# Optimization experiments

Measured on AMD Instinct MI355X. Metric: run time of the kernel, lower is better.

## Reference

```python
import jax, jax.numpy as jnp
import numpy as np

N_POINTS = 2_000_000
N_BATCH = 8


def cart2polar(xyz):
    rho = jnp.sqrt(xyz[:, 0] ** 2 + xyz[:, 1] ** 2)
    phi = jnp.arctan2(xyz[:, 1], xyz[:, 0])
    return jnp.stack((rho, phi, xyz[:, 2]), axis=1)


def setup_inputs() -> dict:
    key = jax.random.key(0)
    k1, k2, k3, k4 = jax.random.split(key, 4)
    xy = jax.random.uniform(k1, (N_POINTS, 2), minval=-50.0, maxval=50.0)
    z = jax.random.uniform(k2, (N_POINTS, 1), minval=-4.0, maxval=2.0)
    inten = jax.random.uniform(k3, (N_POINTS, 1))
    points = jnp.concatenate([xy, z, inten], axis=1)  # [N, 4]
    batch_idx = jnp.sort(jax.random.randint(k4, (N_POINTS,), 0, N_BATCH)).astype(jnp.int32)
    coors_range_xyz = jnp.array([[0.0, 50.0], [-np.pi, np.pi], [-4.0, 2.0]], dtype=jnp.float32)
    spatial_shape = np.array([480, 360, 32])  # static
    scale_list = np.array([2, 4, 1])          # module appends 1; static
    return dict(points=points, batch_idx=batch_idx,
                coors_range_xyz=coors_range_xyz,
                spatial_shape=spatial_shape, scale_list=scale_list)


def _unique_rows(bxyz, dims):
    # Encode [b, gx, gy, gz] rows into a single int32 key (max 8*480*360*32 ~ 44M).
    key = ((bxyz[:, 0] * dims[0] + bxyz[:, 1]) * dims[1] + bxyz[:, 2]) * dims[2] + bxyz[:, 3]
    order = jnp.argsort(key)
    sk = key[order]
    flags = jnp.concatenate([jnp.ones((1,), bool), sk[1:] != sk[:-1]])
    rank = jnp.cumsum(flags.astype(jnp.int32)) - 1          # unique-id per sorted row
    inv = jnp.zeros_like(rank).at[order].set(rank)           # inverse map, like torch.unique
    # first occurrence of each unique row (all rows with same rank are identical)
    unq = jnp.zeros_like(bxyz).at[rank].set(bxyz[order])     # padded to [N, 4]
    num_unique = rank[-1] + 1
    return unq, inv, num_unique


def reference(points, batch_idx, coors_range_xyz, spatial_shape, scale_list):
    pc = points[:, :3]
    xyz_pol = cart2polar(pc)
    lo = coors_range_xyz[:, 0]
    hi = coors_range_xyz[:, 1]
    crop = hi - lo
    ss_np = np.asarray(spatial_shape)
    outs = []
    for scale in [int(s) for s in np.asarray(scale_list)]:
        cells = jnp.asarray(np.ceil(ss_np / scale) - 1.0, dtype=xyz_pol.dtype)
        grid = jnp.floor((jnp.clip(xyz_pol, lo, hi) - lo) / crop * cells).astype(jnp.int32)
        bxyz = jnp.concatenate([batch_idx[:, None].astype(jnp.int32), grid], axis=1)  # [N,4]
        dims = np.ceil(ss_np / scale).astype(np.int64)
        unq, inv, num = _unique_rows(bxyz, dims)
        # reorder unique coords as [b, z, y, x], cast int32 (torch: unq[:, [0,3,2,1]])
        coors = jnp.concatenate([unq[:, 0:1], unq[:, 3:4], unq[:, 2:3], unq[:, 1:2]], axis=1).astype(jnp.int32)
        outs.extend([bxyz, inv, coors, num])
    return tuple(outs)
```

## Files before the change

kernel.cpp:

```cpp
#include <hip/hip_runtime.h>
#include <cstdint>

#define DI __device__ __forceinline__

constexpr int NPTS       = 2000000;
constexpr int STRIDE_OUT = 18000001;
constexpr int OFF_INV    = 8000000;
constexpr int OFF_COORS  = 10000000;
constexpr int OFF_NUM    = 18000000;

constexpr int R2W  = 172800;
constexpr int R4W  = 21600;
constexpr int R1W  = 1382400;
constexpr int RW0  = 0;
constexpr int RW1  = R2W;
constexpr int RW2  = R2W + R4W;
constexpr int WTOT = R2W + R4W + R1W;
constexpr int NB1  = (WTOT + 1023) / 1024;
constexpr int J2   = 8;
constexpr int P1   = 6;
constexpr int J1   = 4;
constexpr int S1W  = 28800;
constexpr int S1BITS = S1W * 32;

constexpr int NBLK_INV   = (NPTS + 255) / 256;
constexpr int NBLK_INV8  = ((NBLK_INV + 7) / 8) * 8;
constexpr int INV_QUOT   = NBLK_INV8 / 8;
constexpr int NBLK_COORS = (WTOT + 255) / 256;
constexpr int NBLK_TAIL  = (3 * NPTS + 255) / 256;

DI float fmul_s(float a, float b){ float r; asm("v_mul_f32 %0, %1, %2" : "=v"(r) : "v"(a), "v"(b)); return r; }
DI float fadd_s(float a, float b){ float r; asm("v_add_f32 %0, %1, %2" : "=v"(r) : "v"(a), "v"(b)); return r; }

DI void compute_keys(float x, float y, float z, int b, int (&key)[3]) {
  const float PI_F     = 3.14159265358979323846f;
  const float TWO_PI_F = 6.28318530717958647692f;
  float rho = sqrtf(fadd_s(fmul_s(x, x), fmul_s(y, y)));
  float phi = atan2f(y, x);
  float tr = (fminf(fmaxf(rho, 0.0f), 50.0f) - 0.0f) / 50.0f;
  float tp = (fminf(fmaxf(phi, -PI_F), PI_F) + PI_F) / TWO_PI_F;
  float tz = (fminf(fmaxf(z, -4.0f), 2.0f) + 4.0f) / 6.0f;
  constexpr float C0[3] = {239.f, 119.f, 479.f};
  constexpr float C1[3] = {179.f,  89.f, 359.f};
  constexpr float C2[3] = { 15.f,   7.f,  31.f};
  constexpr int   D0[3] = {240, 120, 480};
  constexpr int   D1[3] = {180,  90, 360};
  constexpr int   D2[3] = { 16,   8,  32};
  #pragma unroll
  for (int s = 0; s < 3; ++s) {
    int a0 = (int)floorf(tr * C0[s]);
    int a1 = (int)floorf(tp * C1[s]);
    int a2 = (int)floorf(tz * C2[s]);
    key[s] = ((b * D0[s] + a0) * D1[s] + a1) * D2[s] + a2;
  }
}

__global__ __launch_bounds__(256) void pass_keys(const float4* __restrict__ pts,
                                                 const int* __restrict__ batch, int n,
                                                 int* __restrict__ keys,
                                                 int* __restrict__ bstart) {
  int i = blockIdx.x * 256 + threadIdx.x;
  if (i >= n) return;
  float4 p = pts[i];
  int bi = batch[i];
  int key[3];
  compute_keys(p.x, p.y, p.z, bi, key);
  keys[i] = key[0]; keys[n + i] = key[1]; keys[2 * n + i] = key[2];
  if (i == 0) {
    #pragma unroll 1
    for (int k = 0; k <= bi; ++k) bstart[k] = 0;
  }
  int bnext = (i + 1 < n) ? batch[i + 1] : 8;
  #pragma unroll 1
  for (int k = bi + 1; k <= bnext; ++k) bstart[k] = i + 1;
}

__global__ __launch_bounds__(1024) void hist_all(const int* __restrict__ bstart,
                                                 const int* __restrict__ keys, int n,
                                                 uint32_t* __restrict__ rep2s,
                                                 uint32_t* __restrict__ rep4s,
                                                 uint32_t* __restrict__ rep1s) {
  alignas(16) __shared__ uint32_t bmA[S1W];
  alignas(16) __shared__ uint32_t bmB[2700];
  int t = threadIdx.x;
  int pb = blockIdx.x;
  if (pb < 64) {
    int bv = pb & 7, j = pb >> 3;
    for (int w = t * 4; w < 21600; w += 4096) *reinterpret_cast<uint4*>(bmA + w) = make_uint4(0,0,0,0);
    for (int w = t; w < 2700; w += 1024) bmB[w] = 0;
    __syncthreads();
    int lo = bstart[bv];
    int hi = bstart[bv + 1];
    int sz = hi - lo;
    int s = lo + (int)((long long)sz * j / J2);
    int e = lo + (int)((long long)sz * (j + 1) / J2);
    const int* k0 = keys;
    const int* k1 = keys + n;
    for (int i = s + t; i < e; i += 1024) {
      int ink2 = k0[i] - bv * 691200;
      int ink4 = k1[i] - bv * 86400;
      atomicOr(&bmA[ink2 >> 5], 1u << (ink2 & 31));
      atomicOr(&bmB[ink4 >> 5], 1u << (ink4 & 31));
    }
    __syncthreads();
    uint32_t* d2 = rep2s + (size_t)j * R2W + bv * 21600;
    uint32_t* d4 = rep4s + (size_t)j * R4W + bv * 2700;
    for (int w = t * 4; w < 21600; w += 4096) *reinterpret_cast<uint4*>(d2 + w) = *reinterpret_cast<uint4*>(bmA + w);
    for (int w = t * 4; w < 2700; w += 4096) *reinterpret_cast<uint4*>(d4 + w) = *reinterpret_cast<uint4*>(bmB + w);
  } else {
    int bv = pb & 7;
    int id = (pb - 64) >> 3;
    int j = id / 6, r = id - j * 6;
    int slice = bv * 6 + r;
    for (int w = t * 4; w < S1W; w += 4096) *reinterpret_cast<uint4*>(bmA + w) = make_uint4(0,0,0,0);
    __syncthreads();
    int lo = bstart[bv];
    int hi = bstart[bv + 1];
    int sz = hi - lo;
    int s = lo + (int)((long long)sz * j / J1);
    int e = lo + (int)((long long)sz * (j + 1) / J1);
    const int* k2 = keys + 2 * n;
    int base = bv * 5529600 + r * S1BITS;
    for (int i = s + t; i < e; i += 1024) {
      int rel = k2[i] - base;
      if ((unsigned)rel < (unsigned)S1BITS) atomicOr(&bmA[rel >> 5], 1u << (rel & 31));
    }
    __syncthreads();
    uint32_t* d = rep1s + (size_t)j * R1W + (size_t)slice * S1W;
    for (int w = t * 4; w < S1W; w += 4096) *reinterpret_cast<uint4*>(d + w) = *reinterpret_cast<uint4*>(bmA + w);
  }
}

DI uint4 merged_words(int base, const uint32_t* __restrict__ rep2s,
                      const uint32_t* __restrict__ rep4s,
                      const uint32_t* __restrict__ rep1s) {
  uint4 acc = make_uint4(0, 0, 0, 0);
  if (base < RW1) {
    #pragma unroll
    for (int c = 0; c < J2; ++c) {
      uint4 w = *reinterpret_cast<const uint4*>(rep2s + (size_t)c * R2W + base);
      acc.x |= w.x; acc.y |= w.y; acc.z |= w.z; acc.w |= w.w;
    }
  } else if (base < RW2) {
    int l = base - RW1;
    #pragma unroll
    for (int c = 0; c < J2; ++c) {
      uint4 w = *reinterpret_cast<const uint4*>(rep4s + (size_t)c * R4W + l);
      acc.x |= w.x; acc.y |= w.y; acc.z |= w.z; acc.w |= w.w;
    }
  } else {
    int l = base - RW2;
    #pragma unroll
    for (int c = 0; c < J1; ++c) {
      uint4 w = *reinterpret_cast<const uint4*>(rep1s + (size_t)c * R1W + l);
      acc.x |= w.x; acc.y |= w.y; acc.z |= w.z; acc.w |= w.w;
    }
  }
  return acc;
}

__global__ __launch_bounds__(256) void scanA(const uint32_t* __restrict__ rep2s,
                                             const uint32_t* __restrict__ rep4s,
                                             const uint32_t* __restrict__ rep1s,
                                             uint32_t* __restrict__ bits,
                                             uint32_t* __restrict__ blockSums) {
  __shared__ uint32_t lds[256];
  int t = threadIdx.x;
  int base = blockIdx.x * 1024 + t * 4;
  uint32_t s = 0;
  if (base < WTOT) {
    uint4 m = merged_words(base, rep2s, rep4s, rep1s);
    *reinterpret_cast<uint4*>(bits + base) = m;
    s = __popc(m.x) + __popc(m.y) + __popc(m.z) + __popc(m.w);
  }
  lds[t] = s; __syncthreads();
  for (int off = 128; off > 0; off >>= 1) { if (t < off) lds[t] += lds[t + off]; __syncthreads(); }
  if (t == 0) blockSums[blockIdx.x] = lds[0];
}

__global__ __launch_bounds__(256) void scanC(const uint32_t* __restrict__ bits,
                                             const uint32_t* __restrict__ blockSums,
                                             uint2* __restrict__ pairs) {
  __shared__ uint32_t lds[256];
  int t = threadIdx.x;
  uint32_t bs = 0;
  for (int k = t; k < (int)blockIdx.x; k += 256) bs += blockSums[k];
  lds[t] = bs; __syncthreads();
  for (int off = 128; off > 0; off >>= 1) { if (t < off) lds[t] += lds[t + off]; __syncthreads(); }
  uint32_t blockBase = lds[0];
  __syncthreads();
  int base = blockIdx.x * 1024 + t * 4;
  uint32_t b[4] = {0,0,0,0}; uint32_t c[4]; uint32_t sum = 0;
  if (base < WTOT) {
    uint4 w = *reinterpret_cast<const uint4*>(bits + base);
    b[0] = w.x; b[1] = w.y; b[2] = w.z; b[3] = w.w;
  }
  #pragma unroll
  for (int k = 0; k < 4; ++k) { c[k] = __popc(b[k]); sum += c[k]; }
  lds[t] = sum; __syncthreads();
  for (int off = 1; off < 256; off <<= 1) {
    uint32_t x = (t >= off) ? lds[t - off] : 0u; __syncthreads();
    lds[t] += x; __syncthreads();
  }
  uint32_t excl = lds[t] - sum + blockBase;
  if (base < WTOT) {
    #pragma unroll
    for (int k = 0; k < 4; ++k) { pairs[base + k] = make_uint2(b[k], excl); excl += c[k]; }
  }
}

template <int S>
DI int4 decode_key(int key) {
  constexpr int D0[3] = {240, 120, 480};
  constexpr int D1[3] = {180,  90, 360};
  constexpr int D2[3] = { 16,   8,  32};
  int a2 = key & (D2[S] - 1);
  int r  = key / D2[S];
  int q  = r / D1[S];
  int a1 = r - q * D1[S];
  int b  = q / D0[S];
  int a0 = q - b * D0[S];
  return make_int4(b, a0, a1, a2);
}

template <int S>
DI void coors_word(int wi_local, uint32_t bits, uint32_t rank, int* __restrict__ coors) {
  int keybase = wi_local * 32;
  while (bits) {
    int j = __builtin_ctz(bits);
    bits &= bits - 1;
    int4 d = decode_key<S>(keybase + j);
    *reinterpret_cast<int4*>(coors + (size_t)rank * 4) = make_int4(d.x, d.w, d.z, d.y);
    ++rank;
  }
}

__global__ __launch_bounds__(256) void epilogue(int n, const uint2* __restrict__ pairs,
                                                const int* __restrict__ keys,
                                                int* __restrict__ out) {
  int b = blockIdx.x;
  int t = threadIdx.x;
  if (b < NBLK_INV8) {
    int l = (b & 7) * INV_QUOT + (b >> 3);
    if (l >= NBLK_INV) return;
    int i = l * 256 + t;
    if (i >= n) return;
    int key[3] = { keys[i], keys[n + i], keys[2 * n + i] };
    constexpr int RW[3] = {RW0, RW1, RW2};
    *reinterpret_cast<int4*>(out + 0 * STRIDE_OUT + i * 4) = decode_key<0>(key[0]);
    *reinterpret_cast<int4*>(out + 1 * STRIDE_OUT + i * 4) = decode_key<1>(key[1]);
    *reinterpret_cast<int4*>(out + 2 * STRIDE_OUT + i * 4) = decode_key<2>(key[2]);
    #pragma unroll
    for (int s = 0; s < 3; ++s) {
      uint2 pr = pairs[RW[s] + (key[s] >> 5)];
      uint32_t base = pr.y - ((s == 0) ? 0u : pairs[RW[s]].y);
      int rank = (int)(base + __popc(pr.x & ((1u << (key[s] & 31)) - 1u)));
      out[s * STRIDE_OUT + OFF_INV + i] = rank;
    }
  } else if (b < NBLK_INV8 + NBLK_COORS) {
    int wi = (b - NBLK_INV8) * 256 + t;
    if (wi >= WTOT) return;
    uint2 pr = pairs[wi];
    if (!pr.x) return;
    if (wi < RW1)      coors_word<0>(wi,       pr.x, pr.y,                 out + 0 * STRIDE_OUT + OFF_COORS);
    else if (wi < RW2) coors_word<1>(wi - RW1, pr.x, pr.y - pairs[RW1].y,  out + 1 * STRIDE_OUT + OFF_COORS);
    else               coors_word<2>(wi - RW2, pr.x, pr.y - pairs[RW2].y,  out + 2 * STRIDE_OUT + OFF_COORS);
  } else {
    int idx = (b - NBLK_INV8 - NBLK_COORS) * 256 + t;
    if (idx >= 3 * n) return;
    int s = 0, i = idx;
    if (i >= 2 * n)  { s = 2; i -= 2 * n; }
    else if (i >= n) { s = 1; i -= n; }
    uint2 last = pairs[WTOT - 1];
    uint32_t total = last.y + (uint32_t)__popc(last.x);
    uint32_t lo = (s == 0) ? 0u : pairs[(s == 1) ? RW1 : RW2].y;
    uint32_t hi = (s == 0) ? pairs[RW1].y : (s == 1) ? pairs[RW2].y : total;
    uint32_t num = hi - lo;
    if (i == 0) out[s * STRIDE_OUT + OFF_NUM] = (int)num;
    if ((uint32_t)i >= num)
      *reinterpret_cast<int4*>(out + s * STRIDE_OUT + OFF_COORS + (size_t)i * 4) = make_int4(0, 0, 0, 0);
  }
}

extern "C" void kernel_launch(void* const* d_in, const int* in_sizes, int n_in,
                              void* d_out, int out_size, void* d_ws, size_t ws_size,
                              hipStream_t stream) {
  const float4* pts   = (const float4*)d_in[0];
  const int*    batch = (const int*)d_in[1];
  int n = in_sizes[1];
  int* out = (int*)d_out;

  uint32_t* rep2s     = (uint32_t*)d_ws;
  uint32_t* rep4s     = rep2s + (size_t)J2 * R2W;
  uint32_t* rep1s     = rep4s + (size_t)J2 * R4W;
  uint32_t* bits      = rep1s + (size_t)J1 * R1W;
  uint2*    pairs     = (uint2*)(bits + WTOT);
  uint32_t* blockSums = (uint32_t*)(pairs + WTOT);
  int*      bstart    = (int*)(blockSums + NB1);
  int*      keys      = (int*)(bstart + 16);

  int nblk = (n + 255) / 256;
  pass_keys<<<nblk, 256, 0, stream>>>(pts, batch, n, keys, bstart);
  hist_all<<<256, 1024, 0, stream>>>(bstart, keys, n, rep2s, rep4s, rep1s);
  scanA<<<NB1, 256, 0, stream>>>(rep2s, rep4s, rep1s, bits, blockSums);
  scanC<<<NB1, 256, 0, stream>>>(bits, blockSums, pairs);
  epilogue<<<NBLK_INV8 + NBLK_COORS + NBLK_TAIL, 256, 0, stream>>>(n, pairs, keys, out);
}
```

Baseline: 328.2 us.

## Compute inverse ranks from LDS-staged prefix slices and write bxyz in key pass

The bxyz grid rows are now written straight from the key-computation kernel, so the epilogue no longer decodes keys back into coordinates. Inverse-index ranks move into a new kernel where each block stages one slice of the bitmap/prefix pairs in LDS. The block then scans its batch's points and resolves only the keys that fall in that slice, replacing scattered global gathers. The cost is that each point's key is read by every slice block of its batch, and there is one extra kernel launch.

```diff
diff --git a/kernel.cpp b/kernel.cpp
--- a/kernel.cpp
+++ b/kernel.cpp
@@ -18,28 +18,39 @@
 constexpr int WTOT = R2W + R4W + R1W;
 constexpr int NB1  = (WTOT + 1023) / 1024;
 constexpr int J2   = 8;
-constexpr int P1   = 6;
 constexpr int J1   = 4;
 constexpr int S1W  = 28800;
 constexpr int S1BITS = S1W * 32;
 
-constexpr int NBLK_INV   = (NPTS + 255) / 256;
-constexpr int NBLK_INV8  = ((NBLK_INV + 7) / 8) * 8;
-constexpr int INV_QUOT   = NBLK_INV8 / 8;
+constexpr int SLW    = 7200;
+constexpr int SLBITS = SLW * 32;
+constexpr int S4W    = 2700;
+constexpr int NBF    = 8 * 24 * 2;
+constexpr int NB2    = 8 * 3 * 2;
+constexpr int NB4    = 8 * 2;
+
 constexpr int NBLK_COORS = (WTOT + 255) / 256;
 constexpr int NBLK_TAIL  = (3 * NPTS + 255) / 256;
 
 DI float fmul_s(float a, float b){ float r; asm("v_mul_f32 %0, %1, %2" : "=v"(r) : "v"(a), "v"(b)); return r; }
 DI float fadd_s(float a, float b){ float r; asm("v_add_f32 %0, %1, %2" : "=v"(r) : "v"(a), "v"(b)); return r; }
 
-DI void compute_keys(float x, float y, float z, int b, int (&key)[3]) {
+__global__ __launch_bounds__(256) void pass_keys(const float4* __restrict__ pts,
+                                                 const int* __restrict__ batch, int n,
+                                                 int* __restrict__ keys,
+                                                 int* __restrict__ bstart,
+                                                 int* __restrict__ out) {
+  int i = blockIdx.x * 256 + threadIdx.x;
+  if (i >= n) return;
+  float4 p = pts[i];
+  int bi = batch[i];
   const float PI_F     = 3.14159265358979323846f;
   const float TWO_PI_F = 6.28318530717958647692f;
-  float rho = sqrtf(fadd_s(fmul_s(x, x), fmul_s(y, y)));
-  float phi = atan2f(y, x);
+  float rho = sqrtf(fadd_s(fmul_s(p.x, p.x), fmul_s(p.y, p.y)));
+  float phi = atan2f(p.y, p.x);
   float tr = (fminf(fmaxf(rho, 0.0f), 50.0f) - 0.0f) / 50.0f;
   float tp = (fminf(fmaxf(phi, -PI_F), PI_F) + PI_F) / TWO_PI_F;
-  float tz = (fminf(fmaxf(z, -4.0f), 2.0f) + 4.0f) / 6.0f;
+  float tz = (fminf(fmaxf(p.z, -4.0f), 2.0f) + 4.0f) / 6.0f;
   constexpr float C0[3] = {239.f, 119.f, 479.f};
   constexpr float C1[3] = {179.f,  89.f, 359.f};
   constexpr float C2[3] = { 15.f,   7.f,  31.f};
@@ -51,21 +62,9 @@
     int a0 = (int)floorf(tr * C0[s]);
     int a1 = (int)floorf(tp * C1[s]);
     int a2 = (int)floorf(tz * C2[s]);
-    key[s] = ((b * D0[s] + a0) * D1[s] + a1) * D2[s] + a2;
-  }
-}
-
-__global__ __launch_bounds__(256) void pass_keys(const float4* __restrict__ pts,
-                                                 const int* __restrict__ batch, int n,
-                                                 int* __restrict__ keys,
-                                                 int* __restrict__ bstart) {
-  int i = blockIdx.x * 256 + threadIdx.x;
-  if (i >= n) return;
-  float4 p = pts[i];
-  int bi = batch[i];
-  int key[3];
-  compute_keys(p.x, p.y, p.z, bi, key);
-  keys[i] = key[0]; keys[n + i] = key[1]; keys[2 * n + i] = key[2];
+    keys[s * n + i] = ((bi * D0[s] + a0) * D1[s] + a1) * D2[s] + a2;
+    *reinterpret_cast<int4*>(out + s * STRIDE_OUT + i * 4) = make_int4(bi, a0, a1, a2);
+  }
   if (i == 0) {
     #pragma unroll 1
     for (int k = 0; k <= bi; ++k) bstart[k] = 0;
@@ -209,6 +208,74 @@
   }
 }
 
+__global__ __launch_bounds__(512) void inv_lds(const int* __restrict__ bstart,
+                                               const int* __restrict__ keys, int n,
+                                               const uint2* __restrict__ pairs,
+                                               int* __restrict__ out) {
+  alignas(16) __shared__ uint2 lds2[SLW];
+  int t = threadIdx.x;
+  int pb = blockIdx.x;
+  int bv = pb & 7;
+  int lo = bstart[bv], hi = bstart[bv + 1], sz = hi - lo;
+  if (pb < NBF) {
+    int slot = pb >> 3;
+    int r = slot >> 1, j = slot & 1;
+    int gbase = RW2 + bv * 172800 + r * SLW;
+    for (int w = t * 2; w < SLW; w += 1024)
+      *reinterpret_cast<uint4*>(lds2 + w) = *reinterpret_cast<const uint4*>(pairs + gbase + w);
+    uint32_t sub = pairs[RW2].y;
+    __syncthreads();
+    int s0 = lo + (int)((long long)sz * j / 2);
+    int e0 = lo + (int)((long long)sz * (j + 1) / 2);
+    const int* k2 = keys + 2 * n;
+    int basebits = bv * 5529600 + r * SLBITS;
+    int* dst = out + 2 * STRIDE_OUT + OFF_INV;
+    for (int i = s0 + t; i < e0; i += 512) {
+      int rel = k2[i] - basebits;
+      if ((unsigned)rel < (unsigned)SLBITS) {
+        uint2 pr = lds2[rel >> 5];
+        dst[i] = (int)(pr.y - sub + __popc(pr.x & ((1u << (rel & 31)) - 1u)));
+      }
+    }
+  } else if (pb < NBF + NB2) {
+    int slot = (pb - NBF) >> 3;
+    int r = slot >> 1, j = slot & 1;
+    int gbase = RW0 + bv * 21600 + r * SLW;
+    for (int w = t * 2; w < SLW; w += 1024)
+      *reinterpret_cast<uint4*>(lds2 + w) = *reinterpret_cast<const uint4*>(pairs + gbase + w);
+    __syncthreads();
+    int s0 = lo + (int)((long long)sz * j / 2);
+    int e0 = lo + (int)((long long)sz * (j + 1) / 2);
+    const int* k0 = keys;
+    int basebits = bv * 691200 + r * SLBITS;
+    int* dst = out + 0 * STRIDE_OUT + OFF_INV;
+    for (int i = s0 + t; i < e0; i += 512) {
+      int rel = k0[i] - basebits;
+      if ((unsigned)rel < (unsigned)SLBITS) {
+        uint2 pr = lds2[rel >> 5];
+        dst[i] = (int)(pr.y + __popc(pr.x & ((1u << (rel & 31)) - 1u)));
+      }
+    }
+  } else {
+    int j = (pb - NBF - NB2) >> 3;
+    int gbase = RW1 + bv * S4W;
+    for (int w = t * 2; w < S4W; w += 1024)
+      *reinterpret_cast<uint4*>(lds2 + w) = *reinterpret_cast<const uint4*>(pairs + gbase + w);
+    uint32_t sub = pairs[RW1].y;
+    __syncthreads();
+    int s0 = lo + (int)((long long)sz * j / 2);
+    int e0 = lo + (int)((long long)sz * (j + 1) / 2);
+    const int* k1 = keys + n;
+    int basebits = bv * 86400;
+    int* dst = out + 1 * STRIDE_OUT + OFF_INV;
+    for (int i = s0 + t; i < e0; i += 512) {
+      int rel = k1[i] - basebits;
+      uint2 pr = lds2[rel >> 5];
+      dst[i] = (int)(pr.y - sub + __popc(pr.x & ((1u << (rel & 31)) - 1u)));
+    }
+  }
+}
+
 template <int S>
 DI int4 decode_key(int key) {
   constexpr int D0[3] = {240, 120, 480};
@@ -235,30 +302,12 @@
   }
 }
 
-__global__ __launch_bounds__(256) void epilogue(int n, const uint2* __restrict__ pairs,
-                                                const int* __restrict__ keys,
-                                                int* __restrict__ out) {
+__global__ __launch_bounds__(256) void epilogue2(int n, const uint2* __restrict__ pairs,
+                                                 int* __restrict__ out) {
   int b = blockIdx.x;
   int t = threadIdx.x;
-  if (b < NBLK_INV8) {
-    int l = (b & 7) * INV_QUOT + (b >> 3);
-    if (l >= NBLK_INV) return;
-    int i = l * 256 + t;
-    if (i >= n) return;
-    int key[3] = { keys[i], keys[n + i], keys[2 * n + i] };
-    constexpr int RW[3] = {RW0, RW1, RW2};
-    *reinterpret_cast<int4*>(out + 0 * STRIDE_OUT + i * 4) = decode_key<0>(key[0]);
-    *reinterpret_cast<int4*>(out + 1 * STRIDE_OUT + i * 4) = decode_key<1>(key[1]);
-    *reinterpret_cast<int4*>(out + 2 * STRIDE_OUT + i * 4) = decode_key<2>(key[2]);
-    #pragma unroll
-    for (int s = 0; s < 3; ++s) {
-      uint2 pr = pairs[RW[s] + (key[s] >> 5)];
-      uint32_t base = pr.y - ((s == 0) ? 0u : pairs[RW[s]].y);
-      int rank = (int)(base + __popc(pr.x & ((1u << (key[s] & 31)) - 1u)));
-      out[s * STRIDE_OUT + OFF_INV + i] = rank;
-    }
-  } else if (b < NBLK_INV8 + NBLK_COORS) {
-    int wi = (b - NBLK_INV8) * 256 + t;
+  if (b < NBLK_COORS) {
+    int wi = b * 256 + t;
     if (wi >= WTOT) return;
     uint2 pr = pairs[wi];
     if (!pr.x) return;
@@ -266,7 +315,7 @@
     else if (wi < RW2) coors_word<1>(wi - RW1, pr.x, pr.y - pairs[RW1].y,  out + 1 * STRIDE_OUT + OFF_COORS);
     else               coors_word<2>(wi - RW2, pr.x, pr.y - pairs[RW2].y,  out + 2 * STRIDE_OUT + OFF_COORS);
   } else {
-    int idx = (b - NBLK_INV8 - NBLK_COORS) * 256 + t;
+    int idx = (b - NBLK_COORS) * 256 + t;
     if (idx >= 3 * n) return;
     int s = 0, i = idx;
     if (i >= 2 * n)  { s = 2; i -= 2 * n; }
@@ -300,9 +349,10 @@
   int*      keys      = (int*)(bstart + 16);
 
   int nblk = (n + 255) / 256;
-  pass_keys<<<nblk, 256, 0, stream>>>(pts, batch, n, keys, bstart);
+  pass_keys<<<nblk, 256, 0, stream>>>(pts, batch, n, keys, bstart, out);
   hist_all<<<256, 1024, 0, stream>>>(bstart, keys, n, rep2s, rep4s, rep1s);
   scanA<<<NB1, 256, 0, stream>>>(rep2s, rep4s, rep1s, bits, blockSums);
   scanC<<<NB1, 256, 0, stream>>>(bits, blockSums, pairs);
-  epilogue<<<NBLK_INV8 + NBLK_COORS + NBLK_TAIL, 256, 0, stream>>>(n, pairs, keys, out);
-}
+  inv_lds<<<448, 512, 0, stream>>>(bstart, keys, n, pairs, out);
+  epilogue2<<<NBLK_COORS + NBLK_TAIL, 256, 0, stream>>>(n, pairs, out);
+}
```

After: 404.6 us. +23.3%, slower.

## Fuse all five stages into one cooperative persistent kernel with grid syncs

Applied to the files above, without the earlier changes.

Replaces the five separate launches (key computation, bitmap histogram, two scan passes, epilogue) with one cooperative kernel of 256 blocks of 1024 threads that separates the phases with grid-wide barriers. The scan is re-chunked to 4096 words per block and the tail zero-fill runs as a grid-stride loop. The aim is to remove launch gaps and inter-kernel drains. In exchange, the elementwise phases now run with only 256 resident blocks, which may leave them short of latency hiding, and each grid.sync adds barrier cost.

```diff
diff --git a/kernel.cpp b/kernel.cpp
--- a/kernel.cpp
+++ b/kernel.cpp
@@ -1,5 +1,8 @@
 #include <hip/hip_runtime.h>
+#include <hip/hip_cooperative_groups.h>
 #include <cstdint>
+
+namespace cg = cooperative_groups;
 
 #define DI __device__ __forceinline__
 
@@ -16,120 +19,23 @@
 constexpr int RW1  = R2W;
 constexpr int RW2  = R2W + R4W;
 constexpr int WTOT = R2W + R4W + R1W;
-constexpr int NB1  = (WTOT + 1023) / 1024;
 constexpr int J2   = 8;
-constexpr int P1   = 6;
 constexpr int J1   = 4;
 constexpr int S1W  = 28800;
 constexpr int S1BITS = S1W * 32;
 
-constexpr int NBLK_INV   = (NPTS + 255) / 256;
-constexpr int NBLK_INV8  = ((NBLK_INV + 7) / 8) * 8;
-constexpr int INV_QUOT   = NBLK_INV8 / 8;
-constexpr int NBLK_COORS = (WTOT + 255) / 256;
-constexpr int NBLK_TAIL  = (3 * NPTS + 255) / 256;
+constexpr int NBLK = 256;
+constexpr int NTHR = 1024;
+constexpr int NT   = NBLK * NTHR;
+constexpr int CHW  = NTHR * 4;
+constexpr int NCH  = (WTOT + CHW - 1) / CHW;
+
+constexpr int NV   = (NPTS + NTHR - 1) / NTHR;
+constexpr int NV8  = ((NV + 7) / 8) * 8;
+constexpr int VQ   = NV8 / 8;
 
 DI float fmul_s(float a, float b){ float r; asm("v_mul_f32 %0, %1, %2" : "=v"(r) : "v"(a), "v"(b)); return r; }
 DI float fadd_s(float a, float b){ float r; asm("v_add_f32 %0, %1, %2" : "=v"(r) : "v"(a), "v"(b)); return r; }
-
-DI void compute_keys(float x, float y, float z, int b, int (&key)[3]) {
-  const float PI_F     = 3.14159265358979323846f;
-  const float TWO_PI_F = 6.28318530717958647692f;
-  float rho = sqrtf(fadd_s(fmul_s(x, x), fmul_s(y, y)));
-  float phi = atan2f(y, x);
-  float tr = (fminf(fmaxf(rho, 0.0f), 50.0f) - 0.0f) / 50.0f;
-  float tp = (fminf(fmaxf(phi, -PI_F), PI_F) + PI_F) / TWO_PI_F;
-  float tz = (fminf(fmaxf(z, -4.0f), 2.0f) + 4.0f) / 6.0f;
-  constexpr float C0[3] = {239.f, 119.f, 479.f};
-  constexpr float C1[3] = {179.f,  89.f, 359.f};
-  constexpr float C2[3] = { 15.f,   7.f,  31.f};
-  constexpr int   D0[3] = {240, 120, 480};
-  constexpr int   D1[3] = {180,  90, 360};
-  constexpr int   D2[3] = { 16,   8,  32};
-  #pragma unroll
-  for (int s = 0; s < 3; ++s) {
-    int a0 = (int)floorf(tr * C0[s]);
-    int a1 = (int)floorf(tp * C1[s]);
-    int a2 = (int)floorf(tz * C2[s]);
-    key[s] = ((b * D0[s] + a0) * D1[s] + a1) * D2[s] + a2;
-  }
-}
-
-__global__ __launch_bounds__(256) void pass_keys(const float4* __restrict__ pts,
-                                                 const int* __restrict__ batch, int n,
-                                                 int* __restrict__ keys,
-                                                 int* __restrict__ bstart) {
-  int i = blockIdx.x * 256 + threadIdx.x;
-  if (i >= n) return;
-  float4 p = pts[i];
-  int bi = batch[i];
-  int key[3];
-  compute_keys(p.x, p.y, p.z, bi, key);
-  keys[i] = key[0]; keys[n + i] = key[1]; keys[2 * n + i] = key[2];
-  if (i == 0) {
-    #pragma unroll 1
-    for (int k = 0; k <= bi; ++k) bstart[k] = 0;
-  }
-  int bnext = (i + 1 < n) ? batch[i + 1] : 8;
-  #pragma unroll 1
-  for (int k = bi + 1; k <= bnext; ++k) bstart[k] = i + 1;
-}
-
-__global__ __launch_bounds__(1024) void hist_all(const int* __restrict__ bstart,
-                                                 const int* __restrict__ keys, int n,
-                                                 uint32_t* __restrict__ rep2s,
-                                                 uint32_t* __restrict__ rep4s,
-                                                 uint32_t* __restrict__ rep1s) {
-  alignas(16) __shared__ uint32_t bmA[S1W];
-  alignas(16) __shared__ uint32_t bmB[2700];
-  int t = threadIdx.x;
-  int pb = blockIdx.x;
-  if (pb < 64) {
-    int bv = pb & 7, j = pb >> 3;
-    for (int w = t * 4; w < 21600; w += 4096) *reinterpret_cast<uint4*>(bmA + w) = make_uint4(0,0,0,0);
-    for (int w = t; w < 2700; w += 1024) bmB[w] = 0;
-    __syncthreads();
-    int lo = bstart[bv];
-    int hi = bstart[bv + 1];
-    int sz = hi - lo;
-    int s = lo + (int)((long long)sz * j / J2);
-    int e = lo + (int)((long long)sz * (j + 1) / J2);
-    const int* k0 = keys;
-    const int* k1 = keys + n;
-    for (int i = s + t; i < e; i += 1024) {
-      int ink2 = k0[i] - bv * 691200;
-      int ink4 = k1[i] - bv * 86400;
-      atomicOr(&bmA[ink2 >> 5], 1u << (ink2 & 31));
-      atomicOr(&bmB[ink4 >> 5], 1u << (ink4 & 31));
-    }
-    __syncthreads();
-    uint32_t* d2 = rep2s + (size_t)j * R2W + bv * 21600;
-    uint32_t* d4 = rep4s + (size_t)j * R4W + bv * 2700;
-    for (int w = t * 4; w < 21600; w += 4096) *reinterpret_cast<uint4*>(d2 + w) = *reinterpret_cast<uint4*>(bmA + w);
-    for (int w = t * 4; w < 2700; w += 4096) *reinterpret_cast<uint4*>(d4 + w) = *reinterpret_cast<uint4*>(bmB + w);
-  } else {
-    int bv = pb & 7;
-    int id = (pb - 64) >> 3;
-    int j = id / 6, r = id - j * 6;
-    int slice = bv * 6 + r;
-    for (int w = t * 4; w < S1W; w += 4096) *reinterpret_cast<uint4*>(bmA + w) = make_uint4(0,0,0,0);
-    __syncthreads();
-    int lo = bstart[bv];
-    int hi = bstart[bv + 1];
-    int sz = hi - lo;
-    int s = lo + (int)((long long)sz * j / J1);
-    int e = lo + (int)((long long)sz * (j + 1) / J1);
-    const int* k2 = keys + 2 * n;
-    int base = bv * 5529600 + r * S1BITS;
-    for (int i = s + t; i < e; i += 1024) {
-      int rel = k2[i] - base;
-      if ((unsigned)rel < (unsigned)S1BITS) atomicOr(&bmA[rel >> 5], 1u << (rel & 31));
-    }
-    __syncthreads();
-    uint32_t* d = rep1s + (size_t)j * R1W + (size_t)slice * S1W;
-    for (int w = t * 4; w < S1W; w += 4096) *reinterpret_cast<uint4*>(d + w) = *reinterpret_cast<uint4*>(bmA + w);
-  }
-}
 
 DI uint4 merged_words(int base, const uint32_t* __restrict__ rep2s,
                       const uint32_t* __restrict__ rep4s,
@@ -157,56 +63,6 @@
     }
   }
   return acc;
-}
-
-__global__ __launch_bounds__(256) void scanA(const uint32_t* __restrict__ rep2s,
-                                             const uint32_t* __restrict__ rep4s,
-                                             const uint32_t* __restrict__ rep1s,
-                                             uint32_t* __restrict__ bits,
-                                             uint32_t* __restrict__ blockSums) {
-  __shared__ uint32_t lds[256];
-  int t = threadIdx.x;
-  int base = blockIdx.x * 1024 + t * 4;
-  uint32_t s = 0;
-  if (base < WTOT) {
-    uint4 m = merged_words(base, rep2s, rep4s, rep1s);
-    *reinterpret_cast<uint4*>(bits + base) = m;
-    s = __popc(m.x) + __popc(m.y) + __popc(m.z) + __popc(m.w);
-  }
-  lds[t] = s; __syncthreads();
-  for (int off = 128; off > 0; off >>= 1) { if (t < off) lds[t] += lds[t + off]; __syncthreads(); }
-  if (t == 0) blockSums[blockIdx.x] = lds[0];
-}
-
-__global__ __launch_bounds__(256) void scanC(const uint32_t* __restrict__ bits,
-                                             const uint32_t* __restrict__ blockSums,
-                                             uint2* __restrict__ pairs) {
-  __shared__ uint32_t lds[256];
-  int t = threadIdx.x;
-  uint32_t bs = 0;
-  for (int k = t; k < (int)blockIdx.x; k += 256) bs += blockSums[k];
-  lds[t] = bs; __syncthreads();
-  for (int off = 128; off > 0; off >>= 1) { if (t < off) lds[t] += lds[t + off]; __syncthreads(); }
-  uint32_t blockBase = lds[0];
-  __syncthreads();
-  int base = blockIdx.x * 1024 + t * 4;
-  uint32_t b[4] = {0,0,0,0}; uint32_t c[4]; uint32_t sum = 0;
-  if (base < WTOT) {
-    uint4 w = *reinterpret_cast<const uint4*>(bits + base);
-    b[0] = w.x; b[1] = w.y; b[2] = w.z; b[3] = w.w;
-  }
-  #pragma unroll
-  for (int k = 0; k < 4; ++k) { c[k] = __popc(b[k]); sum += c[k]; }
-  lds[t] = sum; __syncthreads();
-  for (int off = 1; off < 256; off <<= 1) {
-    uint32_t x = (t >= off) ? lds[t - off] : 0u; __syncthreads();
-    lds[t] += x; __syncthreads();
-  }
-  uint32_t excl = lds[t] - sum + blockBase;
-  if (base < WTOT) {
-    #pragma unroll
-    for (int k = 0; k < 4; ++k) { pairs[base + k] = make_uint2(b[k], excl); excl += c[k]; }
-  }
 }
 
 template <int S>
@@ -235,50 +91,210 @@
   }
 }
 
-__global__ __launch_bounds__(256) void epilogue(int n, const uint2* __restrict__ pairs,
-                                                const int* __restrict__ keys,
-                                                int* __restrict__ out) {
-  int b = blockIdx.x;
-  int t = threadIdx.x;
-  if (b < NBLK_INV8) {
-    int l = (b & 7) * INV_QUOT + (b >> 3);
-    if (l >= NBLK_INV) return;
-    int i = l * 256 + t;
-    if (i >= n) return;
-    int key[3] = { keys[i], keys[n + i], keys[2 * n + i] };
-    constexpr int RW[3] = {RW0, RW1, RW2};
-    *reinterpret_cast<int4*>(out + 0 * STRIDE_OUT + i * 4) = decode_key<0>(key[0]);
-    *reinterpret_cast<int4*>(out + 1 * STRIDE_OUT + i * 4) = decode_key<1>(key[1]);
-    *reinterpret_cast<int4*>(out + 2 * STRIDE_OUT + i * 4) = decode_key<2>(key[2]);
+__global__ __launch_bounds__(NTHR) void fused(const float4* __restrict__ pts,
+                                              const int* __restrict__ batch, int n,
+                                              int* __restrict__ keys,
+                                              int* __restrict__ bstart,
+                                              uint32_t* __restrict__ rep2s,
+                                              uint32_t* __restrict__ rep4s,
+                                              uint32_t* __restrict__ rep1s,
+                                              uint32_t* __restrict__ bits,
+                                              uint32_t* __restrict__ chunkSums,
+                                              uint2* __restrict__ pairs,
+                                              int* __restrict__ out) {
+  cg::grid_group grid = cg::this_grid();
+  alignas(16) __shared__ uint32_t bmA[S1W];
+  alignas(16) __shared__ uint32_t bmB[2700];
+  const int t = threadIdx.x;
+  const int gtid = (int)blockIdx.x * NTHR + t;
+
+  {
+    const float PI_F     = 3.14159265358979323846f;
+    const float TWO_PI_F = 6.28318530717958647692f;
+    constexpr float C0[3] = {239.f, 119.f, 479.f};
+    constexpr float C1[3] = {179.f,  89.f, 359.f};
+    constexpr float C2[3] = { 15.f,   7.f,  31.f};
+    constexpr int   D0[3] = {240, 120, 480};
+    constexpr int   D1[3] = {180,  90, 360};
+    constexpr int   D2[3] = { 16,   8,  32};
+    for (int i = gtid; i < n; i += NT) {
+      float4 p = pts[i];
+      int bi = batch[i];
+      float rho = sqrtf(fadd_s(fmul_s(p.x, p.x), fmul_s(p.y, p.y)));
+      float phi = atan2f(p.y, p.x);
+      float tr = (fminf(fmaxf(rho, 0.0f), 50.0f) - 0.0f) / 50.0f;
+      float tp = (fminf(fmaxf(phi, -PI_F), PI_F) + PI_F) / TWO_PI_F;
+      float tz = (fminf(fmaxf(p.z, -4.0f), 2.0f) + 4.0f) / 6.0f;
+      #pragma unroll
+      for (int s = 0; s < 3; ++s) {
+        int a0 = (int)floorf(tr * C0[s]);
+        int a1 = (int)floorf(tp * C1[s]);
+        int a2 = (int)floorf(tz * C2[s]);
+        keys[s * n + i] = ((bi * D0[s] + a0) * D1[s] + a1) * D2[s] + a2;
+      }
+      if (i == 0) {
+        #pragma unroll 1
+        for (int k = 0; k <= bi; ++k) bstart[k] = 0;
+      }
+      int bnext = (i + 1 < n) ? batch[i + 1] : 8;
+      #pragma unroll 1
+      for (int k = bi + 1; k <= bnext; ++k) bstart[k] = i + 1;
+    }
+  }
+  grid.sync();
+
+  {
+    int pb = (int)blockIdx.x;
+    if (pb < 64) {
+      int bv = pb & 7, j = pb >> 3;
+      for (int w = t * 4; w < 21600; w += 4096) *reinterpret_cast<uint4*>(bmA + w) = make_uint4(0,0,0,0);
+      for (int w = t; w < 2700; w += 1024) bmB[w] = 0;
+      __syncthreads();
+      int lo = bstart[bv];
+      int hi = bstart[bv + 1];
+      int sz = hi - lo;
+      int s = lo + (int)((long long)sz * j / J2);
+      int e = lo + (int)((long long)sz * (j + 1) / J2);
+      const int* k0 = keys;
+      const int* k1 = keys + n;
+      for (int i = s + t; i < e; i += 1024) {
+        int ink2 = k0[i] - bv * 691200;
+        int ink4 = k1[i] - bv * 86400;
+        atomicOr(&bmA[ink2 >> 5], 1u << (ink2 & 31));
+        atomicOr(&bmB[ink4 >> 5], 1u << (ink4 & 31));
+      }
+      __syncthreads();
+      uint32_t* d2 = rep2s + (size_t)j * R2W + bv * 21600;
+      uint32_t* d4 = rep4s + (size_t)j * R4W + bv * 2700;
+      for (int w = t * 4; w < 21600; w += 4096) *reinterpret_cast<uint4*>(d2 + w) = *reinterpret_cast<uint4*>(bmA + w);
+      for (int w = t * 4; w < 2700; w += 4096) *reinterpret_cast<uint4*>(d4 + w) = *reinterpret_cast<uint4*>(bmB + w);
+    } else {
+      int bv = pb & 7;
+      int id = (pb - 64) >> 3;
+      int j = id / 6, r = id - j * 6;
+      int slice = bv * 6 + r;
+      for (int w = t * 4; w < S1W; w += 4096) *reinterpret_cast<uint4*>(bmA + w) = make_uint4(0,0,0,0);
+      __syncthreads();
+      int lo = bstart[bv];
+      int hi = bstart[bv + 1];
+      int sz = hi - lo;
+      int s = lo + (int)((long long)sz * j / J1);
+      int e = lo + (int)((long long)sz * (j + 1) / J1);
+      const int* k2 = keys + 2 * n;
+      int base = bv * 5529600 + r * S1BITS;
+      for (int i = s + t; i < e; i += 1024) {
+        int rel = k2[i] - base;
+        if ((unsigned)rel < (unsigned)S1BITS) atomicOr(&bmA[rel >> 5], 1u << (rel & 31));
+      }
+      __syncthreads();
+      uint32_t* d = rep1s + (size_t)j * R1W + (size_t)slice * S1W;
+      for (int w = t * 4; w < S1W; w += 4096) *reinterpret_cast<uint4*>(d + w) = *reinterpret_cast<uint4*>(bmA + w);
+    }
+  }
+  grid.sync();
+
+  for (int v = (int)blockIdx.x; v < NCH; v += NBLK) {
+    int base = v * CHW + t * 4;
+    uint32_t s = 0;
+    if (base < WTOT) {
+      uint4 m = merged_words(base, rep2s, rep4s, rep1s);
+      *reinterpret_cast<uint4*>(bits + base) = m;
+      s = __popc(m.x) + __popc(m.y) + __popc(m.z) + __popc(m.w);
+    }
+    __syncthreads();
+    bmA[t] = s;
+    __syncthreads();
+    for (int off = 512; off > 0; off >>= 1) { if (t < off) bmA[t] += bmA[t + off]; __syncthreads(); }
+    if (t == 0) chunkSums[v] = bmA[0];
+  }
+  grid.sync();
+
+  for (int v = (int)blockIdx.x; v < NCH; v += NBLK) {
+    uint32_t bs = (t < v) ? chunkSums[t] : 0u;
+    __syncthreads();
+    bmA[t] = bs;
+    __syncthreads();
+    for (int off = 512; off > 0; off >>= 1) { if (t < off) bmA[t] += bmA[t + off]; __syncthreads(); }
+    uint32_t chunkBase = bmA[0];
+    __syncthreads();
+    int base = v * CHW + t * 4;
+    uint32_t b4[4] = {0,0,0,0}; uint32_t c4[4]; uint32_t sum = 0;
+    if (base < WTOT) {
+      uint4 w = *reinterpret_cast<const uint4*>(bits + base);
+      b4[0] = w.x; b4[1] = w.y; b4[2] = w.z; b4[3] = w.w;
+    }
     #pragma unroll
-    for (int s = 0; s < 3; ++s) {
-      uint2 pr = pairs[RW[s] + (key[s] >> 5)];
-      uint32_t base = pr.y - ((s == 0) ? 0u : pairs[RW[s]].y);
-      int rank = (int)(base + __popc(pr.x & ((1u << (key[s] & 31)) - 1u)));
-      out[s * STRIDE_OUT + OFF_INV + i] = rank;
-    }
-  } else if (b < NBLK_INV8 + NBLK_COORS) {
-    int wi = (b - NBLK_INV8) * 256 + t;
-    if (wi >= WTOT) return;
-    uint2 pr = pairs[wi];
-    if (!pr.x) return;
-    if (wi < RW1)      coors_word<0>(wi,       pr.x, pr.y,                 out + 0 * STRIDE_OUT + OFF_COORS);
-    else if (wi < RW2) coors_word<1>(wi - RW1, pr.x, pr.y - pairs[RW1].y,  out + 1 * STRIDE_OUT + OFF_COORS);
-    else               coors_word<2>(wi - RW2, pr.x, pr.y - pairs[RW2].y,  out + 2 * STRIDE_OUT + OFF_COORS);
-  } else {
-    int idx = (b - NBLK_INV8 - NBLK_COORS) * 256 + t;
-    if (idx >= 3 * n) return;
-    int s = 0, i = idx;
-    if (i >= 2 * n)  { s = 2; i -= 2 * n; }
-    else if (i >= n) { s = 1; i -= n; }
+    for (int k = 0; k < 4; ++k) { c4[k] = __popc(b4[k]); sum += c4[k]; }
+    bmA[t] = sum;
+    __syncthreads();
+    for (int off = 1; off < 1024; off <<= 1) {
+      uint32_t x = (t >= off) ? bmA[t - off] : 0u;
+      __syncthreads();
+      bmA[t] += x;
+      __syncthreads();
+    }
+    uint32_t excl = bmA[t] - sum + chunkBase;
+    if (base < WTOT) {
+      #pragma unroll
+      for (int k = 0; k < 4; ++k) { pairs[base + k] = make_uint2(b4[k], excl); excl += c4[k]; }
+    }
+    __syncthreads();
+  }
+  grid.sync();
+
+  {
+    uint32_t subs1 = pairs[RW1].y;
+    uint32_t subs2 = pairs[RW2].y;
+
+    for (int vb = (int)blockIdx.x; vb < NV8; vb += NBLK) {
+      int lv = (vb & 7) * VQ + (vb >> 3);
+      if (lv >= NV) continue;
+      int i = lv * NTHR + t;
+      if (i >= n) continue;
+      int k0v = keys[i], k1v = keys[n + i], k2v = keys[2 * n + i];
+      *reinterpret_cast<int4*>(out + 0 * STRIDE_OUT + (size_t)i * 4) = decode_key<0>(k0v);
+      *reinterpret_cast<int4*>(out + 1 * STRIDE_OUT + (size_t)i * 4) = decode_key<1>(k1v);
+      *reinterpret_cast<int4*>(out + 2 * STRIDE_OUT + (size_t)i * 4) = decode_key<2>(k2v);
+      {
+        uint2 pr = pairs[RW0 + (k0v >> 5)];
+        out[0 * STRIDE_OUT + OFF_INV + i] = (int)(pr.y + __popc(pr.x & ((1u << (k0v & 31)) - 1u)));
+      }
+      {
+        uint2 pr = pairs[RW1 + (k1v >> 5)];
+        out[1 * STRIDE_OUT + OFF_INV + i] = (int)(pr.y - subs1 + __popc(pr.x & ((1u << (k1v & 31)) - 1u)));
+      }
+      {
+        uint2 pr = pairs[RW2 + (k2v >> 5)];
+        out[2 * STRIDE_OUT + OFF_INV + i] = (int)(pr.y - subs2 + __popc(pr.x & ((1u << (k2v & 31)) - 1u)));
+      }
+    }
+
+    for (int wi = gtid; wi < WTOT; wi += NT) {
+      uint2 pr = pairs[wi];
+      if (!pr.x) continue;
+      if (wi < RW1)      coors_word<0>(wi,       pr.x, pr.y,         out + 0 * STRIDE_OUT + OFF_COORS);
+      else if (wi < RW2) coors_word<1>(wi - RW1, pr.x, pr.y - subs1, out + 1 * STRIDE_OUT + OFF_COORS);
+      else               coors_word<2>(wi - RW2, pr.x, pr.y - subs2, out + 2 * STRIDE_OUT + OFF_COORS);
+    }
+
     uint2 last = pairs[WTOT - 1];
     uint32_t total = last.y + (uint32_t)__popc(last.x);
-    uint32_t lo = (s == 0) ? 0u : pairs[(s == 1) ? RW1 : RW2].y;
-    uint32_t hi = (s == 0) ? pairs[RW1].y : (s == 1) ? pairs[RW2].y : total;
-    uint32_t num = hi - lo;
-    if (i == 0) out[s * STRIDE_OUT + OFF_NUM] = (int)num;
-    if ((uint32_t)i >= num)
-      *reinterpret_cast<int4*>(out + s * STRIDE_OUT + OFF_COORS + (size_t)i * 4) = make_int4(0, 0, 0, 0);
+    uint32_t num0 = subs1;
+    uint32_t num1 = subs2 - subs1;
+    uint32_t num2 = total - subs2;
+    if (gtid == 0) {
+      out[0 * STRIDE_OUT + OFF_NUM] = (int)num0;
+      out[1 * STRIDE_OUT + OFF_NUM] = (int)num1;
+      out[2 * STRIDE_OUT + OFF_NUM] = (int)num2;
+    }
+    for (int idx = gtid; idx < 3 * n; idx += NT) {
+      int s = 0, i = idx;
+      if (i >= 2 * n)  { s = 2; i -= 2 * n; }
+      else if (i >= n) { s = 1; i -= n; }
+      uint32_t num = (s == 0) ? num0 : (s == 1) ? num1 : num2;
+      if ((uint32_t)i >= num)
+        *reinterpret_cast<int4*>(out + s * STRIDE_OUT + OFF_COORS + (size_t)i * 4) = make_int4(0, 0, 0, 0);
+    }
   }
 }
 
@@ -295,14 +311,13 @@
   uint32_t* rep1s     = rep4s + (size_t)J2 * R4W;
   uint32_t* bits      = rep1s + (size_t)J1 * R1W;
   uint2*    pairs     = (uint2*)(bits + WTOT);
-  uint32_t* blockSums = (uint32_t*)(pairs + WTOT);
-  int*      bstart    = (int*)(blockSums + NB1);
+  uint32_t* chunkSums = (uint32_t*)(pairs + WTOT);
+  int*      bstart    = (int*)(chunkSums + NCH + 15);
   int*      keys      = (int*)(bstart + 16);
 
-  int nblk = (n + 255) / 256;
-  pass_keys<<<nblk, 256, 0, stream>>>(pts, batch, n, keys, bstart);
-  hist_all<<<256, 1024, 0, stream>>>(bstart, keys, n, rep2s, rep4s, rep1s);
-  scanA<<<NB1, 256, 0, stream>>>(rep2s, rep4s, rep1s, bits, blockSums);
-  scanC<<<NB1, 256, 0, stream>>>(bits, blockSums, pairs);
-  epilogue<<<NBLK_INV8 + NBLK_COORS + NBLK_TAIL, 256, 0, stream>>>(n, pairs, keys, out);
-}
+  void* args[12] = { (void*)&pts, (void*)&batch, (void*)&n, (void*)&keys, (void*)&bstart,
+                     (void*)&rep2s, (void*)&rep4s, (void*)&rep1s, (void*)&bits,
+                     (void*)&chunkSums, (void*)&pairs, (void*)&out };
+  hipLaunchCooperativeKernel(reinterpret_cast<void*>(fused), dim3(NBLK), dim3(NTHR),
+                             args, 0, stream);
+}
```

After: 499.3 us. 52.1% more time.

## Write bxyz grid outputs in key pass and unroll histogram and inverse loops

Applied to the files above, without the earlier changes.

The per-point [b,gx,gy,gz] grid rows are now written directly in the key-computation kernel instead of being decoded from keys in the epilogue. The histogram loops are unrolled by four so more independent key loads and LDS atomics are in flight. The inverse-rank epilogue blocks now handle four points per thread, batching key and pair loads before the rank writes. This shifts output write traffic earlier and cuts decode work, but adds register pressure and a larger, more divergent pass_keys kernel.

```diff
diff --git a/kernel.cpp b/kernel.cpp
--- a/kernel.cpp
+++ b/kernel.cpp
@@ -18,28 +18,35 @@
 constexpr int WTOT = R2W + R4W + R1W;
 constexpr int NB1  = (WTOT + 1023) / 1024;
 constexpr int J2   = 8;
-constexpr int P1   = 6;
 constexpr int J1   = 4;
 constexpr int S1W  = 28800;
 constexpr int S1BITS = S1W * 32;
 
-constexpr int NBLK_INV   = (NPTS + 255) / 256;
-constexpr int NBLK_INV8  = ((NBLK_INV + 7) / 8) * 8;
-constexpr int INV_QUOT   = NBLK_INV8 / 8;
+constexpr int NBLK_INVU  = (NPTS + 1023) / 1024;
+constexpr int NBLK_INVUP = ((NBLK_INVU + 7) / 8) * 8;
+constexpr int IVQ        = NBLK_INVUP / 8;
 constexpr int NBLK_COORS = (WTOT + 255) / 256;
 constexpr int NBLK_TAIL  = (3 * NPTS + 255) / 256;
 
 DI float fmul_s(float a, float b){ float r; asm("v_mul_f32 %0, %1, %2" : "=v"(r) : "v"(a), "v"(b)); return r; }
 DI float fadd_s(float a, float b){ float r; asm("v_add_f32 %0, %1, %2" : "=v"(r) : "v"(a), "v"(b)); return r; }
 
-DI void compute_keys(float x, float y, float z, int b, int (&key)[3]) {
+__global__ __launch_bounds__(256) void pass_keys(const float4* __restrict__ pts,
+                                                 const int* __restrict__ batch, int n,
+                                                 int* __restrict__ keys,
+                                                 int* __restrict__ bstart,
+                                                 int* __restrict__ out) {
+  int i = blockIdx.x * 256 + threadIdx.x;
+  if (i >= n) return;
+  float4 p = pts[i];
+  int bi = batch[i];
   const float PI_F     = 3.14159265358979323846f;
   const float TWO_PI_F = 6.28318530717958647692f;
-  float rho = sqrtf(fadd_s(fmul_s(x, x), fmul_s(y, y)));
-  float phi = atan2f(y, x);
+  float rho = sqrtf(fadd_s(fmul_s(p.x, p.x), fmul_s(p.y, p.y)));
+  float phi = atan2f(p.y, p.x);
   float tr = (fminf(fmaxf(rho, 0.0f), 50.0f) - 0.0f) / 50.0f;
   float tp = (fminf(fmaxf(phi, -PI_F), PI_F) + PI_F) / TWO_PI_F;
-  float tz = (fminf(fmaxf(z, -4.0f), 2.0f) + 4.0f) / 6.0f;
+  float tz = (fminf(fmaxf(p.z, -4.0f), 2.0f) + 4.0f) / 6.0f;
   constexpr float C0[3] = {239.f, 119.f, 479.f};
   constexpr float C1[3] = {179.f,  89.f, 359.f};
   constexpr float C2[3] = { 15.f,   7.f,  31.f};
@@ -51,21 +58,9 @@
     int a0 = (int)floorf(tr * C0[s]);
     int a1 = (int)floorf(tp * C1[s]);
     int a2 = (int)floorf(tz * C2[s]);
-    key[s] = ((b * D0[s] + a0) * D1[s] + a1) * D2[s] + a2;
-  }
-}
-
-__global__ __launch_bounds__(256) void pass_keys(const float4* __restrict__ pts,
-                                                 const int* __restrict__ batch, int n,
-                                                 int* __restrict__ keys,
-                                                 int* __restrict__ bstart) {
-  int i = blockIdx.x * 256 + threadIdx.x;
-  if (i >= n) return;
-  float4 p = pts[i];
-  int bi = batch[i];
-  int key[3];
-  compute_keys(p.x, p.y, p.z, bi, key);
-  keys[i] = key[0]; keys[n + i] = key[1]; keys[2 * n + i] = key[2];
+    keys[s * n + i] = ((bi * D0[s] + a0) * D1[s] + a1) * D2[s] + a2;
+    *reinterpret_cast<int4*>(out + s * STRIDE_OUT + (size_t)i * 4) = make_int4(bi, a0, a1, a2);
+  }
   if (i == 0) {
     #pragma unroll 1
     for (int k = 0; k <= bi; ++k) bstart[k] = 0;
@@ -96,9 +91,26 @@
     int e = lo + (int)((long long)sz * (j + 1) / J2);
     const int* k0 = keys;
     const int* k1 = keys + n;
-    for (int i = s + t; i < e; i += 1024) {
-      int ink2 = k0[i] - bv * 691200;
-      int ink4 = k1[i] - bv * 86400;
+    int b2 = bv * 691200;
+    int b4 = bv * 86400;
+    int i = s + t;
+    for (; i < e - 3072; i += 4096) {
+      int a0 = k0[i], a1 = k0[i + 1024], a2 = k0[i + 2048], a3 = k0[i + 3072];
+      int c0 = k1[i], c1 = k1[i + 1024], c2 = k1[i + 2048], c3 = k1[i + 3072];
+      int x0 = a0 - b2, x1 = a1 - b2, x2 = a2 - b2, x3 = a3 - b2;
+      int y0 = c0 - b4, y1 = c1 - b4, y2 = c2 - b4, y3 = c3 - b4;
+      atomicOr(&bmA[x0 >> 5], 1u << (x0 & 31));
+      atomicOr(&bmA[x1 >> 5], 1u << (x1 & 31));
+      atomicOr(&bmA[x2 >> 5], 1u << (x2 & 31));
+      atomicOr(&bmA[x3 >> 5], 1u << (x3 & 31));
+      atomicOr(&bmB[y0 >> 5], 1u << (y0 & 31));
+      atomicOr(&bmB[y1 >> 5], 1u << (y1 & 31));
+      atomicOr(&bmB[y2 >> 5], 1u << (y2 & 31));
+      atomicOr(&bmB[y3 >> 5], 1u << (y3 & 31));
+    }
+    for (; i < e; i += 1024) {
+      int ink2 = k0[i] - b2;
+      int ink4 = k1[i] - b4;
       atomicOr(&bmA[ink2 >> 5], 1u << (ink2 & 31));
       atomicOr(&bmB[ink4 >> 5], 1u << (ink4 & 31));
     }
@@ -121,7 +133,16 @@
     int e = lo + (int)((long long)sz * (j + 1) / J1);
     const int* k2 = keys + 2 * n;
     int base = bv * 5529600 + r * S1BITS;
-    for (int i = s + t; i < e; i += 1024) {
+    int i = s + t;
+    for (; i < e - 3072; i += 4096) {
+      int r0 = k2[i] - base, r1 = k2[i + 1024] - base;
+      int r2 = k2[i + 2048] - base, r3 = k2[i + 3072] - base;
+      if ((unsigned)r0 < (unsigned)S1BITS) atomicOr(&bmA[r0 >> 5], 1u << (r0 & 31));
+      if ((unsigned)r1 < (unsigned)S1BITS) atomicOr(&bmA[r1 >> 5], 1u << (r1 & 31));
+      if ((unsigned)r2 < (unsigned)S1BITS) atomicOr(&bmA[r2 >> 5], 1u << (r2 & 31));
+      if ((unsigned)r3 < (unsigned)S1BITS) atomicOr(&bmA[r3 >> 5], 1u << (r3 & 31));
+    }
+    for (; i < e; i += 1024) {
       int rel = k2[i] - base;
       if ((unsigned)rel < (unsigned)S1BITS) atomicOr(&bmA[rel >> 5], 1u << (rel & 31));
     }
@@ -240,25 +261,43 @@
                                                 int* __restrict__ out) {
   int b = blockIdx.x;
   int t = threadIdx.x;
-  if (b < NBLK_INV8) {
-    int l = (b & 7) * INV_QUOT + (b >> 3);
-    if (l >= NBLK_INV) return;
-    int i = l * 256 + t;
-    if (i >= n) return;
-    int key[3] = { keys[i], keys[n + i], keys[2 * n + i] };
-    constexpr int RW[3] = {RW0, RW1, RW2};
-    *reinterpret_cast<int4*>(out + 0 * STRIDE_OUT + i * 4) = decode_key<0>(key[0]);
-    *reinterpret_cast<int4*>(out + 1 * STRIDE_OUT + i * 4) = decode_key<1>(key[1]);
-    *reinterpret_cast<int4*>(out + 2 * STRIDE_OUT + i * 4) = decode_key<2>(key[2]);
-    #pragma unroll
-    for (int s = 0; s < 3; ++s) {
-      uint2 pr = pairs[RW[s] + (key[s] >> 5)];
-      uint32_t base = pr.y - ((s == 0) ? 0u : pairs[RW[s]].y);
-      int rank = (int)(base + __popc(pr.x & ((1u << (key[s] & 31)) - 1u)));
-      out[s * STRIDE_OUT + OFF_INV + i] = rank;
-    }
-  } else if (b < NBLK_INV8 + NBLK_COORS) {
-    int wi = (b - NBLK_INV8) * 256 + t;
+  if (b < NBLK_INVUP) {
+    int lv = (b & 7) * IVQ + (b >> 3);
+    if (lv >= NBLK_INVU) return;
+    int i0 = lv * 1024 + t;
+    uint32_t subs1 = pairs[RW1].y;
+    uint32_t subs2 = pairs[RW2].y;
+    int kv[3][4];
+    bool ok[4];
+    #pragma unroll
+    for (int u = 0; u < 4; ++u) {
+      int i = i0 + u * 256;
+      ok[u] = (i < n);
+      int ii = ok[u] ? i : 0;
+      kv[0][u] = keys[ii];
+      kv[1][u] = keys[n + ii];
+      kv[2][u] = keys[2 * n + ii];
+    }
+    uint2 pr[3][4];
+    #pragma unroll
+    for (int u = 0; u < 4; ++u) {
+      pr[0][u] = pairs[RW0 + (kv[0][u] >> 5)];
+      pr[1][u] = pairs[RW1 + (kv[1][u] >> 5)];
+      pr[2][u] = pairs[RW2 + (kv[2][u] >> 5)];
+    }
+    #pragma unroll
+    for (int u = 0; u < 4; ++u) {
+      if (!ok[u]) continue;
+      int i = i0 + u * 256;
+      out[0 * STRIDE_OUT + OFF_INV + i] =
+          (int)(pr[0][u].y + __popc(pr[0][u].x & ((1u << (kv[0][u] & 31)) - 1u)));
+      out[1 * STRIDE_OUT + OFF_INV + i] =
+          (int)(pr[1][u].y - subs1 + __popc(pr[1][u].x & ((1u << (kv[1][u] & 31)) - 1u)));
+      out[2 * STRIDE_OUT + OFF_INV + i] =
+          (int)(pr[2][u].y - subs2 + __popc(pr[2][u].x & ((1u << (kv[2][u] & 31)) - 1u)));
+    }
+  } else if (b < NBLK_INVUP + NBLK_COORS) {
+    int wi = (b - NBLK_INVUP) * 256 + t;
     if (wi >= WTOT) return;
     uint2 pr = pairs[wi];
     if (!pr.x) return;
@@ -266,7 +305,7 @@
     else if (wi < RW2) coors_word<1>(wi - RW1, pr.x, pr.y - pairs[RW1].y,  out + 1 * STRIDE_OUT + OFF_COORS);
     else               coors_word<2>(wi - RW2, pr.x, pr.y - pairs[RW2].y,  out + 2 * STRIDE_OUT + OFF_COORS);
   } else {
-    int idx = (b - NBLK_INV8 - NBLK_COORS) * 256 + t;
+    int idx = (b - NBLK_INVUP - NBLK_COORS) * 256 + t;
     if (idx >= 3 * n) return;
     int s = 0, i = idx;
     if (i >= 2 * n)  { s = 2; i -= 2 * n; }
@@ -300,9 +339,9 @@
   int*      keys      = (int*)(bstart + 16);
 
   int nblk = (n + 255) / 256;
-  pass_keys<<<nblk, 256, 0, stream>>>(pts, batch, n, keys, bstart);
+  pass_keys<<<nblk, 256, 0, stream>>>(pts, batch, n, keys, bstart, out);
   hist_all<<<256, 1024, 0, stream>>>(bstart, keys, n, rep2s, rep4s, rep1s);
   scanA<<<NB1, 256, 0, stream>>>(rep2s, rep4s, rep1s, bits, blockSums);
   scanC<<<NB1, 256, 0, stream>>>(bits, blockSums, pairs);
-  epilogue<<<NBLK_INV8 + NBLK_COORS + NBLK_TAIL, 256, 0, stream>>>(n, pairs, keys, out);
-}
+  epilogue<<<NBLK_INVUP + NBLK_COORS + NBLK_TAIL, 256, 0, stream>>>(n, pairs, keys, out);
+}
```

Measured after the change: 333.8 us. No clear change (+1.7%).
